# Kernel optimization log

Measured on AMD Instinct MI355X. Metric: run time of the kernel, lower is better.

The kernel has to match this reference:

```python
import jax, jax.numpy as jnp
import numpy as np


def setup_inputs() -> dict:
    key = jax.random.key(0)
    ks = jax.random.split(key, 10)
    N1, N2, F, D, E = 50000, 50000, 1024, 128, 1000000
    s = 0.02
    return {
        "x_gene": jax.random.normal(ks[0], (N1, F), jnp.float32),
        "x_cell": jax.random.normal(ks[1], (N2, F), jnp.float32),
        "edge_label_index": jax.random.randint(ks[2], (2, E), 0, N1, jnp.int64 if jax.config.jax_enable_x64 else jnp.int32),
        "W1": jax.random.normal(ks[3], (F, D), jnp.float32) * s,
        "b1": jnp.zeros((D,), jnp.float32),
        "W2": jax.random.normal(ks[4], (F, D), jnp.float32) * s,
        "b2": jnp.zeros((D,), jnp.float32),
        "Wm1": jax.random.normal(ks[5], (2 * D, 64), jnp.float32) * s,
        "bm1": jnp.zeros((64,), jnp.float32),
        "Wm2": jax.random.normal(ks[6], (64, 32), jnp.float32) * s,
        "bm2": jnp.zeros((32,), jnp.float32),
        "Wm3": jax.random.normal(ks[7], (32, 1), jnp.float32) * s,
        "bm3": jnp.zeros((1,), jnp.float32),
    }


def reference(x_gene, x_cell, edge_label_index, W1, b1, W2, b2, Wm1, bm1, Wm2, bm2, Wm3, bm3):
    # Node-type linear projections (dropout is identity in eval mode)
    h1 = x_gene @ W1 + b1          # [N1, D]
    h2 = x_cell @ W2 + b2          # [N2, D]
    # Edge gather + concat
    ef = jnp.concatenate([h1[edge_label_index[0]], h2[edge_label_index[1]]], axis=-1)  # [E, 2D]
    # 3-layer MLP classifier
    h = jax.nn.relu(ef @ Wm1 + bm1)
    h = jax.nn.relu(h @ Wm2 + bm2)
    pred = (h @ Wm3 + bm3)[..., 0]  # squeeze(-1) -> [E]
    return pred
```

## Files before the change

kernel.cpp:

```cpp
#include <hip/hip_runtime.h>
#include <hip/hip_bf16.h>
#include <stdint.h>

typedef __attribute__((ext_vector_type(8))) short short8;
typedef __attribute__((ext_vector_type(4))) float float4v;

__device__ __forceinline__ float bf2f(uint16_t u) {
    union { uint32_t i; float f; } v; v.i = ((uint32_t)u) << 16; return v.f;
}
__device__ __forceinline__ uint16_t f2bf(float f) {
    union { float f; uint32_t i; } v; v.f = f;
    uint32_t x = v.i;
    uint32_t r = (x + 0x7fffu + ((x >> 16) & 1u)) >> 16;
    return (uint16_t)r;
}
__device__ __forceinline__ float relu_nanprop(float x) {
    return 0.5f * (x + fabsf(x));
}

__global__ __launch_bounds__(256) void precompute_kernel(
    const float* __restrict__ W1, const float* __restrict__ W2,
    const float* __restrict__ Wm1,
    const float* __restrict__ b1, const float* __restrict__ b2,
    const float* __restrict__ bm1,
    uint16_t* __restrict__ A1T, uint16_t* __restrict__ A2T,
    float* __restrict__ tbias)
{
    int b = blockIdx.x, t = threadIdx.x;
    if (b < 512) {
        int g   = b * 256 + t;
        int mat = g >> 16;
        int rem = g & 65535;
        int n   = rem >> 10;
        int f   = rem & 1023;
        const float* W  = mat ? W2 : W1;
        const float* wm = Wm1 + mat * 128 * 64;
        const float4* Wrow = (const float4*)(W + (size_t)f * 128);
        float acc = 0.f;
        #pragma unroll
        for (int c = 0; c < 32; ++c) {
            float4 w = Wrow[c];
            acc += w.x * wm[(c * 4 + 0) * 64 + n];
            acc += w.y * wm[(c * 4 + 1) * 64 + n];
            acc += w.z * wm[(c * 4 + 2) * 64 + n];
            acc += w.w * wm[(c * 4 + 3) * 64 + n];
        }
        (mat ? A2T : A1T)[(size_t)n * 1024 + f] = f2bf(acc);
    } else if (t < 64) {
        float acc = bm1[t];
        for (int d = 0; d < 128; ++d) acc += b1[d] * Wm1[d * 64 + t];
        for (int d = 0; d < 128; ++d) acc += b2[d] * Wm1[(128 + d) * 64 + t];
        tbias[t] = acc;
    }
}

__global__ __launch_bounds__(256) void gemm64_kernel(
    const float* __restrict__ X1, const float* __restrict__ X2,
    const uint16_t* __restrict__ A1T, const uint16_t* __restrict__ A2T,
    uint16_t* __restrict__ G1, uint16_t* __restrict__ G2, int M1, int M2)
{
    const int which = blockIdx.y;
    const float* __restrict__ X     = which ? X2  : X1;
    const uint16_t* __restrict__ BT = which ? A2T : A1T;
    uint16_t* __restrict__ G        = which ? G2  : G1;
    const int M = which ? M2 : M1;

    const int blockRow = blockIdx.x * 128;
    if (blockRow >= M) return;

    __shared__ uint16_t As[128 * 64];

    const int t    = threadIdx.x;
    const int wid  = t >> 6;
    const int lane = t & 63;
    const int m    = lane & 15;
    const int q    = lane >> 4;

    float4v acc[2][4];
    #pragma unroll
    for (int r = 0; r < 2; ++r)
        #pragma unroll
        for (int nt = 0; nt < 4; ++nt)
            acc[r][nt] = (float4v){0.f, 0.f, 0.f, 0.f};

    for (int kk = 0; kk < 16; ++kk) {
        float4 av0[4], av1[4];
        int    dstc[4];
        #pragma unroll
        for (int it = 0; it < 4; ++it) {
            int c   = it * 256 + t;
            int row = c >> 3, pc = c & 7;
            int lc  = pc ^ (row & 7);
            int grow = blockRow + row; if (grow >= M) grow = M - 1;
            const float4* src = (const float4*)(X + (size_t)grow * 1024 + kk * 64 + lc * 8);
            av0[it] = src[0];
            av1[it] = src[1];
            dstc[it] = c * 8;
        }
        __syncthreads();
        #pragma unroll
        for (int it = 0; it < 4; ++it) {
            uint4 pk;
            pk.x = (uint32_t)f2bf(av0[it].x) | ((uint32_t)f2bf(av0[it].y) << 16);
            pk.y = (uint32_t)f2bf(av0[it].z) | ((uint32_t)f2bf(av0[it].w) << 16);
            pk.z = (uint32_t)f2bf(av1[it].x) | ((uint32_t)f2bf(av1[it].y) << 16);
            pk.w = (uint32_t)f2bf(av1[it].z) | ((uint32_t)f2bf(av1[it].w) << 16);
            *(uint4*)(As + dstc[it]) = pk;
        }
        __syncthreads();

        #pragma unroll
        for (int s = 0; s < 2; ++s) {
            short8 af[2], bfr[4];
            #pragma unroll
            for (int r = 0; r < 2; ++r) {
                int row = wid * 32 + r * 16 + m;
                int pc  = (s * 4 + q) ^ (row & 7);
                af[r] = *(const short8*)(As + row * 64 + pc * 8);
            }
            #pragma unroll
            for (int nt = 0; nt < 4; ++nt) {
                int n = nt * 16 + m;
                bfr[nt] = *(const short8*)(BT + (size_t)n * 1024 + kk * 64 + (s * 4 + q) * 8);
            }
            #pragma unroll
            for (int r = 0; r < 2; ++r)
                #pragma unroll
                for (int nt = 0; nt < 4; ++nt)
                    acc[r][nt] = __builtin_amdgcn_mfma_f32_16x16x32_bf16(
                        af[r], bfr[nt], acc[r][nt], 0, 0, 0);
        }
    }

    #pragma unroll
    for (int r = 0; r < 2; ++r) {
        #pragma unroll
        for (int reg = 0; reg < 4; ++reg) {
            int grow = blockRow + wid * 32 + r * 16 + q * 4 + reg;
            if (grow < M) {
                #pragma unroll
                for (int nt = 0; nt < 4; ++nt)
                    G[(size_t)grow * 64 + nt * 16 + m] = f2bf(acc[r][nt][reg]);
            }
        }
    }
}

__global__ __launch_bounds__(256) void edge_mlp_kernel(
    const uint16_t* __restrict__ g1, const uint16_t* __restrict__ g2,
    const float* __restrict__ tbias, const int* __restrict__ eidx,
    const float* __restrict__ Wm2, const float* __restrict__ bm2,
    const float* __restrict__ Wm3, const float* __restrict__ bm3,
    float* __restrict__ out, int E)
{
    int e = blockIdx.x * 256 + threadIdx.x;
    if (e >= E) e = E - 1;
    int src = eidx[e];
    int dst = eidx[E + e];
    const uint4* r1 = (const uint4*)(g1 + (size_t)src * 64);
    const uint4* r2 = (const uint4*)(g2 + (size_t)dst * 64);

    float u[32];
    #pragma unroll
    for (int j = 0; j < 32; ++j) u[j] = bm2[j];

    #pragma unroll
    for (int c = 0; c < 8; ++c) {
        uint4 a = r1[c], b = r2[c];
        uint32_t aw[4] = { a.x, a.y, a.z, a.w };
        uint32_t bw[4] = { b.x, b.y, b.z, b.w };
        float tv[8];
        #pragma unroll
        for (int h = 0; h < 4; ++h) {
            float alo, ahi, blo, bhi;
            { union { uint32_t i; float f; } v; v.i = aw[h] << 16;        alo = v.f; }
            { union { uint32_t i; float f; } v; v.i = aw[h] & 0xffff0000u; ahi = v.f; }
            { union { uint32_t i; float f; } v; v.i = bw[h] << 16;        blo = v.f; }
            { union { uint32_t i; float f; } v; v.i = bw[h] & 0xffff0000u; bhi = v.f; }
            tv[2 * h]     = relu_nanprop(alo + blo + tbias[c * 8 + 2 * h]);
            tv[2 * h + 1] = relu_nanprop(ahi + bhi + tbias[c * 8 + 2 * h + 1]);
        }
        #pragma unroll
        for (int i = 0; i < 8; ++i) {
            const float* wrow = Wm2 + (c * 8 + i) * 32;
            #pragma unroll
            for (int j = 0; j < 32; ++j)
                u[j] = fmaf(tv[i], wrow[j], u[j]);
        }
    }

    float p = bm3[0];
    #pragma unroll
    for (int j = 0; j < 32; ++j)
        p += relu_nanprop(u[j]) * Wm3[j];
    out[e] = p;
}

extern "C" void kernel_launch(void* const* d_in, const int* in_sizes, int n_in,
                              void* d_out, int out_size, void* d_ws, size_t ws_size,
                              hipStream_t stream) {
    const float* x_gene = (const float*)d_in[0];
    const float* x_cell = (const float*)d_in[1];
    const int*   eidx   = (const int*)d_in[2];
    const float* W1  = (const float*)d_in[3];
    const float* b1  = (const float*)d_in[4];
    const float* W2  = (const float*)d_in[5];
    const float* b2  = (const float*)d_in[6];
    const float* Wm1 = (const float*)d_in[7];
    const float* bm1 = (const float*)d_in[8];
    const float* Wm2 = (const float*)d_in[9];
    const float* bm2 = (const float*)d_in[10];
    const float* Wm3 = (const float*)d_in[11];
    const float* bm3 = (const float*)d_in[12];

    const int M1 = in_sizes[0] / 1024;
    const int M2 = in_sizes[1] / 1024;
    const int E  = in_sizes[2] / 2;

    uint8_t* ws = (uint8_t*)d_ws;
    uint16_t* A1T   = (uint16_t*)(ws + 0);
    uint16_t* A2T   = (uint16_t*)(ws + 131072);
    float*    tbias = (float*)(ws + 262144);
    uint16_t* G1    = (uint16_t*)(ws + 524288);
    size_t g1_bytes = ((size_t)M1 * 64 * 2 + 127) & ~(size_t)127;
    uint16_t* G2    = (uint16_t*)(ws + 524288 + g1_bytes);

    precompute_kernel<<<513, 256, 0, stream>>>(
        W1, W2, Wm1, b1, b2, bm1, A1T, A2T, tbias);

    int Mmax = M1 > M2 ? M1 : M2;
    dim3 ggrid((Mmax + 127) / 128, 2);
    gemm64_kernel<<<ggrid, 256, 0, stream>>>(x_gene, x_cell, A1T, A2T, G1, G2, M1, M2);

    edge_mlp_kernel<<<(E + 255) / 256, 256, 0, stream>>>(
        G1, G2, tbias, eidx, Wm2, bm2, Wm3, bm3, (float*)d_out, E);
}
```

Baseline: 573.7 us.

## Stream GEMM A operand directly from global with register prefetch, drop LDS staging

The projection GEMM no longer stages X tiles through shared memory behind two barriers. Each wave loads its 16 rows straight from global into registers in MFMA fragment layout, prefetching A two k-steps ahead and B one step ahead, and the block tile shrinks to 64 rows. The aim is to keep the memory-bound fp32 X read streaming without sync stalls. The precompute kernel is reorganised so each wave owns one row f with lanes over n, which gives coalesced Wm1 reads and a broadcast W row, and the edge MLP software-prefetches the next gathered chunk. The risks are a less contiguous per-lane global access pattern for X (32B per lane per row, strided across rows) and higher register pressure.

```diff
diff --git a/kernel.cpp b/kernel.cpp
--- a/kernel.cpp
+++ b/kernel.cpp
@@ -28,23 +28,17 @@
 {
     int b = blockIdx.x, t = threadIdx.x;
     if (b < 512) {
-        int g   = b * 256 + t;
-        int mat = g >> 16;
-        int rem = g & 65535;
-        int n   = rem >> 10;
-        int f   = rem & 1023;
-        const float* W  = mat ? W2 : W1;
-        const float* wm = Wm1 + mat * 128 * 64;
-        const float4* Wrow = (const float4*)(W + (size_t)f * 128);
+        int g   = b * 4 + (t >> 6);
+        int mat = g >> 10;
+        int f   = g & 1023;
+        int n   = t & 63;
+        const float* W    = mat ? W2 : W1;
+        const float* wm   = Wm1 + mat * 128 * 64;
+        const float* Wrow = W + (size_t)f * 128;
         float acc = 0.f;
-        #pragma unroll
-        for (int c = 0; c < 32; ++c) {
-            float4 w = Wrow[c];
-            acc += w.x * wm[(c * 4 + 0) * 64 + n];
-            acc += w.y * wm[(c * 4 + 1) * 64 + n];
-            acc += w.z * wm[(c * 4 + 2) * 64 + n];
-            acc += w.w * wm[(c * 4 + 3) * 64 + n];
-        }
+        #pragma unroll 8
+        for (int d = 0; d < 128; ++d)
+            acc = fmaf(Wrow[d], wm[d * 64 + n], acc);
         (mat ? A2T : A1T)[(size_t)n * 1024 + f] = f2bf(acc);
     } else if (t < 64) {
         float acc = bm1[t];
@@ -54,7 +48,7 @@
     }
 }
 
-__global__ __launch_bounds__(256) void gemm64_kernel(
+__global__ __launch_bounds__(256, 4) void gemm64_kernel(
     const float* __restrict__ X1, const float* __restrict__ X2,
     const uint16_t* __restrict__ A1T, const uint16_t* __restrict__ A2T,
     uint16_t* __restrict__ G1, uint16_t* __restrict__ G2, int M1, int M2)
@@ -65,83 +59,67 @@
     uint16_t* __restrict__ G        = which ? G2  : G1;
     const int M = which ? M2 : M1;
 
-    const int blockRow = blockIdx.x * 128;
-    if (blockRow >= M) return;
-
-    __shared__ uint16_t As[128 * 64];
-
     const int t    = threadIdx.x;
     const int wid  = t >> 6;
     const int lane = t & 63;
     const int m    = lane & 15;
     const int q    = lane >> 4;
 
-    float4v acc[2][4];
-    #pragma unroll
-    for (int r = 0; r < 2; ++r)
-        #pragma unroll
-        for (int nt = 0; nt < 4; ++nt)
-            acc[r][nt] = (float4v){0.f, 0.f, 0.f, 0.f};
-
-    for (int kk = 0; kk < 16; ++kk) {
-        float4 av0[4], av1[4];
-        int    dstc[4];
-        #pragma unroll
-        for (int it = 0; it < 4; ++it) {
-            int c   = it * 256 + t;
-            int row = c >> 3, pc = c & 7;
-            int lc  = pc ^ (row & 7);
-            int grow = blockRow + row; if (grow >= M) grow = M - 1;
-            const float4* src = (const float4*)(X + (size_t)grow * 1024 + kk * 64 + lc * 8);
-            av0[it] = src[0];
-            av1[it] = src[1];
-            dstc[it] = c * 8;
-        }
-        __syncthreads();
-        #pragma unroll
-        for (int it = 0; it < 4; ++it) {
-            uint4 pk;
-            pk.x = (uint32_t)f2bf(av0[it].x) | ((uint32_t)f2bf(av0[it].y) << 16);
-            pk.y = (uint32_t)f2bf(av0[it].z) | ((uint32_t)f2bf(av0[it].w) << 16);
-            pk.z = (uint32_t)f2bf(av1[it].x) | ((uint32_t)f2bf(av1[it].y) << 16);
-            pk.w = (uint32_t)f2bf(av1[it].z) | ((uint32_t)f2bf(av1[it].w) << 16);
-            *(uint4*)(As + dstc[it]) = pk;
-        }
-        __syncthreads();
-
-        #pragma unroll
-        for (int s = 0; s < 2; ++s) {
-            short8 af[2], bfr[4];
+    const int rowBase = blockIdx.x * 64 + wid * 16;
+    if (rowBase >= M) return;
+    int lrow = rowBase + m;
+    if (lrow >= M) lrow = M - 1;
+
+    const float*    Xb = X  + (size_t)lrow * 1024 + q * 8;
+    const uint16_t* Bb = BT + (size_t)m * 1024 + q * 8;
+
+    float4v acc[4];
+    #pragma unroll
+    for (int nt = 0; nt < 4; ++nt) acc[nt] = (float4v){0.f, 0.f, 0.f, 0.f};
+
+    float4 pa0[2], pa1[2];
+    pa0[0] = *(const float4*)(Xb + 0);
+    pa1[0] = *(const float4*)(Xb + 4);
+    pa0[1] = *(const float4*)(Xb + 32);
+    pa1[1] = *(const float4*)(Xb + 36);
+    short8 pb0 = *(const short8*)(Bb + 0 * 16384);
+    short8 pb1 = *(const short8*)(Bb + 1 * 16384);
+    short8 pb2 = *(const short8*)(Bb + 2 * 16384);
+    short8 pb3 = *(const short8*)(Bb + 3 * 16384);
+
+    #pragma unroll
+    for (int p = 0; p < 32; ++p) {
+        float4 a0 = pa0[p & 1], a1 = pa1[p & 1];
+        const int np = (p + 2 < 32) ? p + 2 : p;
+        pa0[p & 1] = *(const float4*)(Xb + 32 * np);
+        pa1[p & 1] = *(const float4*)(Xb + 32 * np + 4);
+
+        short8 b0 = pb0, b1 = pb1, b2 = pb2, b3 = pb3;
+        const int bp = (p + 1 < 32) ? p + 1 : p;
+        pb0 = *(const short8*)(Bb + 0 * 16384 + 32 * bp);
+        pb1 = *(const short8*)(Bb + 1 * 16384 + 32 * bp);
+        pb2 = *(const short8*)(Bb + 2 * 16384 + 32 * bp);
+        pb3 = *(const short8*)(Bb + 3 * 16384 + 32 * bp);
+
+        union { short8 s8; uint32_t u[4]; } P;
+        P.u[0] = (uint32_t)f2bf(a0.x) | ((uint32_t)f2bf(a0.y) << 16);
+        P.u[1] = (uint32_t)f2bf(a0.z) | ((uint32_t)f2bf(a0.w) << 16);
+        P.u[2] = (uint32_t)f2bf(a1.x) | ((uint32_t)f2bf(a1.y) << 16);
+        P.u[3] = (uint32_t)f2bf(a1.z) | ((uint32_t)f2bf(a1.w) << 16);
+
+        acc[0] = __builtin_amdgcn_mfma_f32_16x16x32_bf16(P.s8, b0, acc[0], 0, 0, 0);
+        acc[1] = __builtin_amdgcn_mfma_f32_16x16x32_bf16(P.s8, b1, acc[1], 0, 0, 0);
+        acc[2] = __builtin_amdgcn_mfma_f32_16x16x32_bf16(P.s8, b2, acc[2], 0, 0, 0);
+        acc[3] = __builtin_amdgcn_mfma_f32_16x16x32_bf16(P.s8, b3, acc[3], 0, 0, 0);
+    }
+
+    #pragma unroll
+    for (int reg = 0; reg < 4; ++reg) {
+        int grow = rowBase + q * 4 + reg;
+        if (grow < M) {
             #pragma unroll
-            for (int r = 0; r < 2; ++r) {
-                int row = wid * 32 + r * 16 + m;
-                int pc  = (s * 4 + q) ^ (row & 7);
-                af[r] = *(const short8*)(As + row * 64 + pc * 8);
-            }
-            #pragma unroll
-            for (int nt = 0; nt < 4; ++nt) {
-                int n = nt * 16 + m;
-                bfr[nt] = *(const short8*)(BT + (size_t)n * 1024 + kk * 64 + (s * 4 + q) * 8);
-            }
-            #pragma unroll
-            for (int r = 0; r < 2; ++r)
-                #pragma unroll
-                for (int nt = 0; nt < 4; ++nt)
-                    acc[r][nt] = __builtin_amdgcn_mfma_f32_16x16x32_bf16(
-                        af[r], bfr[nt], acc[r][nt], 0, 0, 0);
-        }
-    }
-
-    #pragma unroll
-    for (int r = 0; r < 2; ++r) {
-        #pragma unroll
-        for (int reg = 0; reg < 4; ++reg) {
-            int grow = blockRow + wid * 32 + r * 16 + q * 4 + reg;
-            if (grow < M) {
-                #pragma unroll
-                for (int nt = 0; nt < 4; ++nt)
-                    G[(size_t)grow * 64 + nt * 16 + m] = f2bf(acc[r][nt][reg]);
-            }
+            for (int nt = 0; nt < 4; ++nt)
+                G[(size_t)grow * 64 + nt * 16 + m] = f2bf(acc[nt][reg]);
         }
     }
 }
@@ -164,9 +142,13 @@
     #pragma unroll
     for (int j = 0; j < 32; ++j) u[j] = bm2[j];
 
+    uint4 a = r1[0], b = r2[0];
+
     #pragma unroll
     for (int c = 0; c < 8; ++c) {
-        uint4 a = r1[c], b = r2[c];
+        const int nc = (c + 1 < 8) ? c + 1 : 7;
+        uint4 na = r1[nc], nb = r2[nc];
+
         uint32_t aw[4] = { a.x, a.y, a.z, a.w };
         uint32_t bw[4] = { b.x, b.y, b.z, b.w };
         float tv[8];
@@ -187,6 +169,7 @@
             for (int j = 0; j < 32; ++j)
                 u[j] = fmaf(tv[i], wrow[j], u[j]);
         }
+        a = na; b = nb;
     }
 
     float p = bm3[0];
@@ -229,7 +212,7 @@
         W1, W2, Wm1, b1, b2, bm1, A1T, A2T, tbias);
 
     int Mmax = M1 > M2 ? M1 : M2;
-    dim3 ggrid((Mmax + 127) / 128, 2);
+    dim3 ggrid((Mmax + 63) / 64, 2);
     gemm64_kernel<<<ggrid, 256, 0, stream>>>(x_gene, x_cell, A1T, A2T, G1, G2, M1, M2);
 
     edge_mlp_kernel<<<(E + 255) / 256, 256, 0, stream>>>(
```

After: 591.9 us. 3.2% more time.
